# Performance work log

Measured on AMD Instinct MI355X. Metric: run time of the kernel, lower is better.

## Reference

```python
import jax, jax.numpy as jnp
import numpy as np

B, S, DM, H, D = 2, 1024, 1024, 16, 64  # batch, seq, d_model, heads, head_dim


def setup_inputs() -> dict:
    key = jax.random.key(0)
    ks = jax.random.split(key, 16)
    sc = 1.0 / np.sqrt(DM)
    scd = 1.0 / np.sqrt(D)
    return {
        "hidden_states": jax.random.normal(ks[0], (B, S, DM), dtype=jnp.float32),
        # frozen base_attn projections
        "Wq": jax.random.normal(ks[1], (DM, DM), dtype=jnp.float32) * sc,
        "bq": jnp.zeros((DM,), dtype=jnp.float32),
        "Wk": jax.random.normal(ks[2], (DM, DM), dtype=jnp.float32) * sc,
        "bk": jnp.zeros((DM,), dtype=jnp.float32),
        "Wv": jax.random.normal(ks[3], (DM, DM), dtype=jnp.float32) * sc,
        "bv": jnp.zeros((DM,), dtype=jnp.float32),
        "Wo": jax.random.normal(ks[4], (DM, DM), dtype=jnp.float32) * sc,
        "bo": jnp.zeros((DM,), dtype=jnp.float32),
        # trainable hedgehog feature maps (per-head Linear(head_dim, head_dim))
        "Wfq": jax.random.normal(ks[5], (D, D), dtype=jnp.float32) * scd,
        "bfq": jnp.zeros((D,), dtype=jnp.float32),
        "Wfk": jax.random.normal(ks[6], (D, D), dtype=jnp.float32) * scd,
        "bfk": jnp.zeros((D,), dtype=jnp.float32),
    }


def _heads(x):
    # (B, S, DM) -> (B, H, S, D)
    return x.reshape(B, S, H, D).transpose(0, 2, 1, 3)


def _feature_map(x, W, b):
    # HedgehogFeatureMap: Linear then concat(exp(x), exp(-x)) along last dim
    y = jnp.einsum('bhsd,ed->bhse', x, W) + b
    return jnp.concatenate([jnp.exp(y), jnp.exp(-y)], axis=-1)  # (B,H,S,2D)


def reference(hidden_states, Wq, bq, Wk, bk, Wv, bv, Wo, bo, Wfq, bfq, Wfk, bfk):
    # base_attn: standard multi-head softmax attention with output_attentions=True
    q = _heads(hidden_states @ Wq.T + bq)
    k = _heads(hidden_states @ Wk.T + bk)
    v = _heads(hidden_states @ Wv.T + bv)
    scores = jnp.einsum('bhmd,bhnd->bhmn', q, k) / jnp.sqrt(jnp.float32(D))
    true_attns = jax.nn.softmax(scores, axis=-1)  # (B,H,S,S)
    ctx = jnp.einsum('bhmn,bhnd->bhmd', true_attns, v)
    outputs = ctx.transpose(0, 2, 1, 3).reshape(B, S, DM) @ Wo.T + bo

    # hedgehog path: feature maps on q/k then sum-normalized quadratic attention
    fq = _feature_map(q, Wfq, bfq)
    fk = _feature_map(k, Wfk, bfk)
    qk = jnp.einsum('bhmd,bhnd->bhmn', fq, fk)
    pred_attns = qk / jnp.sum(qk, axis=-1, keepdims=True)
    return (outputs, pred_attns, true_attns)
```

## Files before the change

### kernel.cpp

```cpp
#include <hip/hip_runtime.h>
#include <math.h>

constexpr int B_ = 2, S_ = 1024, DM_ = 1024, NH_ = 16, HD_ = 64;
constexpr long SD = (long)S_ * DM_;
constexpr long SS = (long)S_ * S_;

typedef _Float16 half8 __attribute__((ext_vector_type(8)));
typedef _Float16 half4 __attribute__((ext_vector_type(4)));
typedef float floatx4 __attribute__((ext_vector_type(4)));

__device__ __forceinline__ void gl_lds16(const void* g, void* l) {
    __builtin_amdgcn_global_load_lds(
        (const __attribute__((address_space(1))) void*)g,
        (__attribute__((address_space(3))) void*)l, 16, 0, 0);
}

__device__ __forceinline__ void nt_store4(const floatx4& v, float* p) {
    __builtin_nontemporal_store(v, (floatx4*)p);
}

__global__ __launch_bounds__(256) void cvt_all(
    const float* __restrict__ hs,  const float* __restrict__ Wq,
    const float* __restrict__ Wk,  const float* __restrict__ Wv,
    const float* __restrict__ Wo,  const float* __restrict__ Wfq,
    const float* __restrict__ Wfk,
    _Float16* __restrict__ hsH, _Float16* __restrict__ WqH,
    _Float16* __restrict__ WkH, _Float16* __restrict__ WvH,
    _Float16* __restrict__ WoH, _Float16* __restrict__ WfqH,
    _Float16* __restrict__ WfkH)
{
    long i = (long)blockIdx.x * 256 + threadIdx.x;
    const float* src; _Float16* dst; long off;
    if (i < 524288)       { src = hs;  dst = hsH;  off = i; }
    else if (i < 786432)  { src = Wq;  dst = WqH;  off = i - 524288; }
    else if (i < 1048576) { src = Wk;  dst = WkH;  off = i - 786432; }
    else if (i < 1310720) { src = Wv;  dst = WvH;  off = i - 1048576; }
    else if (i < 1572864) { src = Wo;  dst = WoH;  off = i - 1310720; }
    else if (i < 1573888) { src = Wfq; dst = WfqH; off = i - 1572864; }
    else                  { src = Wfk; dst = WfkH; off = i - 1573888; }
    float4 v = ((const float4*)src)[off];
    half4 h = { (_Float16)v.x, (_Float16)v.y, (_Float16)v.z, (_Float16)v.w };
    ((half4*)dst)[off] = h;
}

template <int BM, int BN, int WM, int WN>
__global__ __launch_bounds__(256) void mm_nt(
    const _Float16* __restrict__ Ap, const _Float16* __restrict__ Wp,
    const float* __restrict__ bias, const float* __restrict__ skp,
    float* __restrict__ Cf,
    _Float16* __restrict__ Ch, int K, int lda, int ldw, int ldc,
    long sAb, long sAh, long sWb, long sWh, long sCb, long sCh,
    float scale, int mode)
{
    constexpr int MI = WM / 16, NI = WN / 16;
    const int z = blockIdx.z, b = z / NH_, h = z % NH_;
    const int wave = threadIdx.x >> 6, lane = threadIdx.x & 63;
    const int m0 = blockIdx.y * BM, n0 = blockIdx.x * BN;
    const int wm = (wave >> 1) * WM, wn = (wave & 1) * WN;
    const int r16 = lane & 15, quad = lane >> 4;

    const _Float16* Az = Ap + (long)b * sAb + (long)h * sAh;
    const _Float16* Wz = Wp + (long)b * sWb + (long)h * sWh;

    __shared__ __align__(16) _Float16 As[2 * BM * 32];
    __shared__ __align__(16) _Float16 Bs[2 * BN * 32];
    __shared__ float skz[128];
    __shared__ float rsinvs[BM];

    if (skp) {
        if (threadIdx.x < 128) {
            float s = 0.f;
#pragma unroll
            for (int m = 0; m < 16; ++m)
                s += skp[((long)z * 16 + m) * 128 + threadIdx.x];
            skz[threadIdx.x] = s;
        }
        __syncthreads();
        if (threadIdx.x < BM) {
            const _Float16* p = Az + (long)(m0 + threadIdx.x) * lda;
            float acc = 0.f;
#pragma unroll
            for (int d0 = 0; d0 < 128; d0 += 8) {
                half8 v = *(const half8*)(p + d0);
#pragma unroll
                for (int j = 0; j < 8; ++j)
                    acc = fmaf((float)v[j], skz[d0 + j], acc);
            }
            rsinvs[threadIdx.x] = 1.f / acc;
        }
    }

    floatx4 acc[MI][NI];
#pragma unroll
    for (int i = 0; i < MI; ++i)
#pragma unroll
        for (int j = 0; j < NI; ++j)
#pragma unroll
            for (int r = 0; r < 4; ++r) acc[i][j][r] = 0.f;

    for (int k0 = 0; k0 < K; k0 += 64) {
#pragma unroll
        for (int hf = 0; hf < 2; ++hf) {
#pragma unroll
            for (int c = wave * (BM / 64); c < (wave + 1) * (BM / 64); ++c) {
                const _Float16* g = Az + (long)(m0 + c * 16 + (lane >> 2)) * lda
                                    + k0 + hf * 32 + (lane & 3) * 8;
                gl_lds16(g, &As[hf * BM * 32 + c * 512]);
            }
#pragma unroll
            for (int c = wave * (BN / 64); c < (wave + 1) * (BN / 64); ++c) {
                const _Float16* g = Wz + (long)(n0 + c * 16 + (lane >> 2)) * ldw
                                    + k0 + hf * 32 + (lane & 3) * 8;
                gl_lds16(g, &Bs[hf * BN * 32 + c * 512]);
            }
        }
        __syncthreads();

#pragma unroll
        for (int hf = 0; hf < 2; ++hf) {
            half8 af[MI], bf8[NI];
#pragma unroll
            for (int i = 0; i < MI; ++i)
                af[i] = *(const half8*)&As[hf * BM * 32
                                           + (wm + i * 16 + r16) * 32 + quad * 8];
#pragma unroll
            for (int j = 0; j < NI; ++j)
                bf8[j] = *(const half8*)&Bs[hf * BN * 32
                                            + (wn + j * 16 + r16) * 32 + quad * 8];
#pragma unroll
            for (int i = 0; i < MI; ++i)
#pragma unroll
                for (int j = 0; j < NI; ++j)
                    acc[i][j] = __builtin_amdgcn_mfma_f32_16x16x32_f16(
                        bf8[j], af[i], acc[i][j], 0, 0, 0);
        }
        __syncthreads();
    }

    const long cb = (long)b * sCb + (long)h * sCh;
#pragma unroll
    for (int i = 0; i < MI; ++i) {
        const int row = m0 + wm + i * 16 + r16;
        const float rs = skp ? rsinvs[row - m0] : 1.f;
#pragma unroll
        for (int j = 0; j < NI; ++j) {
            const int col = n0 + wn + j * 16 + quad * 4;
            floatx4 v;
#pragma unroll
            for (int r = 0; r < 4; ++r) v[r] = acc[i][j][r] * scale;
            if (bias) {
                float4 bv = *(const float4*)&bias[col];
                v[0] += bv.x; v[1] += bv.y; v[2] += bv.z; v[3] += bv.w;
            }
            if (skp) {
#pragma unroll
                for (int r = 0; r < 4; ++r) v[r] *= rs;
            }
            if (mode == 0) {
                nt_store4(v, &Cf[cb + (long)row * ldc + col]);
            } else {
                half4 hv = { (_Float16)v[0], (_Float16)v[1],
                             (_Float16)v[2], (_Float16)v[3] };
                *(half4*)&Ch[cb + (long)row * ldc + col] = hv;
            }
        }
    }
}

__global__ __launch_bounds__(256) void qkv_proj(
    const _Float16* __restrict__ hsH,
    const _Float16* __restrict__ W0, const _Float16* __restrict__ W1,
    const _Float16* __restrict__ W2,
    const float* __restrict__ b0, const float* __restrict__ b1,
    const float* __restrict__ b2,
    _Float16* __restrict__ QH, _Float16* __restrict__ KH,
    _Float16* __restrict__ VtH)
{
    const int z = blockIdx.z;
    const _Float16* W = (z == 0) ? W0 : (z == 1) ? W1 : W2;
    const float* bias = (z == 0) ? b0 : (z == 1) ? b1 : b2;

    const int wave = threadIdx.x >> 6, lane = threadIdx.x & 63;
    const int m0 = blockIdx.y * 64, n0 = blockIdx.x * 128;
    const int wm = (wave >> 1) * 32, wn = (wave & 1) * 64;
    const int r16 = lane & 15, quad = lane >> 4;

    __shared__ __align__(16) _Float16 As[2 * 64 * 32];
    __shared__ __align__(16) _Float16 Bs[2 * 128 * 32];

    floatx4 acc[2][4];
#pragma unroll
    for (int i = 0; i < 2; ++i)
#pragma unroll
        for (int j = 0; j < 4; ++j)
#pragma unroll
            for (int r = 0; r < 4; ++r) acc[i][j][r] = 0.f;

    for (int k0 = 0; k0 < 1024; k0 += 64) {
#pragma unroll
        for (int hf = 0; hf < 2; ++hf) {
            const _Float16* ga = hsH + (long)(m0 + wave * 16 + (lane >> 2)) * 1024
                                 + k0 + hf * 32 + (lane & 3) * 8;
            gl_lds16(ga, &As[hf * 2048 + wave * 512]);
#pragma unroll
            for (int c = wave * 2; c < wave * 2 + 2; ++c) {
                const _Float16* gb = W + (long)(n0 + c * 16 + (lane >> 2)) * 1024
                                     + k0 + hf * 32 + (lane & 3) * 8;
                gl_lds16(gb, &Bs[hf * 4096 + c * 512]);
            }
        }
        __syncthreads();

#pragma unroll
        for (int hf = 0; hf < 2; ++hf) {
            half8 af[2], bf8[4];
#pragma unroll
            for (int i = 0; i < 2; ++i)
                af[i] = *(const half8*)&As[hf * 2048
                                           + (wm + i * 16 + r16) * 32 + quad * 8];
#pragma unroll
            for (int j = 0; j < 4; ++j)
                bf8[j] = *(const half8*)&Bs[hf * 4096
                                            + (wn + j * 16 + r16) * 32 + quad * 8];
#pragma unroll
            for (int i = 0; i < 2; ++i)
#pragma unroll
                for (int j = 0; j < 4; ++j)
                    acc[i][j] = __builtin_amdgcn_mfma_f32_16x16x32_f16(
                        bf8[j], af[i], acc[i][j], 0, 0, 0);
        }
        __syncthreads();
    }

    _Float16* dst = (z == 0) ? QH : KH;
#pragma unroll
    for (int i = 0; i < 2; ++i) {
        const int row = m0 + wm + i * 16 + r16;
#pragma unroll
        for (int j = 0; j < 4; ++j) {
            const int col = n0 + wn + j * 16 + quad * 4;
            float4 bv = *(const float4*)&bias[col];
            float v0 = acc[i][j][0] + bv.x, v1 = acc[i][j][1] + bv.y;
            float v2 = acc[i][j][2] + bv.z, v3 = acc[i][j][3] + bv.w;
            if (z < 2) {
                half4 hv = { (_Float16)v0, (_Float16)v1,
                             (_Float16)v2, (_Float16)v3 };
                *(half4*)&dst[(long)row * 1024 + col] = hv;
            } else {
                const int bb = row >> 10, s = row & 1023;
                const int hh = col >> 6, d0 = col & 63;
                float vv[4] = { v0, v1, v2, v3 };
#pragma unroll
                for (int r = 0; r < 4; ++r)
                    VtH[((((long)bb * 16 + hh) * 64 + d0 + r) << 10) | s] =
                        (_Float16)vv[r];
            }
        }
    }
}

__global__ __launch_bounds__(512) void attn_fused(
    const _Float16* __restrict__ Q, const _Float16* __restrict__ K,
    const _Float16* __restrict__ Vt, float* __restrict__ trueA,
    _Float16* __restrict__ ctx)
{
    const int z = blockIdx.y, b = z >> 4, h = z & 15;
    const int m0 = blockIdx.x * 32;
    const int wave = threadIdx.x >> 6, lane = threadIdx.x & 63;
    const int r16 = lane & 15, quad = lane >> 4;
    const int c0 = wave * 128;

    __shared__ __align__(16) _Float16 Ps[32 * 1024];
    float* redmx = (float*)Ps;
    float* redsm = (float*)Ps + 256;

    const _Float16* Qb = Q + (long)b * SD + h * 64;
    const _Float16* Kb = K + (long)b * SD + h * 64;

    half8 qf[2][2];
#pragma unroll
    for (int mi = 0; mi < 2; ++mi)
#pragma unroll
        for (int ks = 0; ks < 2; ++ks)
            qf[mi][ks] = *(const half8*)&Qb[(long)(m0 + mi * 16 + r16) * DM_
                                            + ks * 32 + quad * 8];

    floatx4 acc[2][8];
#pragma unroll
    for (int mi = 0; mi < 2; ++mi)
#pragma unroll
        for (int nj = 0; nj < 8; ++nj)
#pragma unroll
            for (int r = 0; r < 4; ++r) acc[mi][nj][r] = 0.f;

#pragma unroll
    for (int ks = 0; ks < 2; ++ks) {
#pragma unroll
        for (int nj = 0; nj < 8; ++nj) {
            half8 kf = *(const half8*)&Kb[(long)(c0 + nj * 16 + r16) * DM_
                                          + ks * 32 + quad * 8];
            acc[0][nj] = __builtin_amdgcn_mfma_f32_16x16x32_f16(
                kf, qf[0][ks], acc[0][nj], 0, 0, 0);
            acc[1][nj] = __builtin_amdgcn_mfma_f32_16x16x32_f16(
                kf, qf[1][ks], acc[1][nj], 0, 0, 0);
        }
    }

    float mxl[2];
#pragma unroll
    for (int mi = 0; mi < 2; ++mi) {
        float m = acc[mi][0][0];
#pragma unroll
        for (int nj = 0; nj < 8; ++nj)
#pragma unroll
            for (int r = 0; r < 4; ++r) m = fmaxf(m, acc[mi][nj][r]);
        m = fmaxf(m, __shfl_xor(m, 16, 64));
        m = fmaxf(m, __shfl_xor(m, 32, 64));
        mxl[mi] = m;
    }
    if (quad == 0) {
        redmx[wave * 32 + r16]      = mxl[0];
        redmx[wave * 32 + 16 + r16] = mxl[1];
    }
    __syncthreads();
    float mx[2];
#pragma unroll
    for (int mi = 0; mi < 2; ++mi) {
        float m = redmx[mi * 16 + r16];
#pragma unroll
        for (int w = 1; w < 8; ++w)
            m = fmaxf(m, redmx[w * 32 + mi * 16 + r16]);
        mx[mi] = m;
    }

    float sml[2];
#pragma unroll
    for (int mi = 0; mi < 2; ++mi) {
        float s = 0.f;
#pragma unroll
        for (int nj = 0; nj < 8; ++nj)
#pragma unroll
            for (int r = 0; r < 4; ++r) {
                float p = __expf((acc[mi][nj][r] - mx[mi]) * 0.125f);
                acc[mi][nj][r] = p;
                s += p;
            }
        s += __shfl_xor(s, 16, 64);
        s += __shfl_xor(s, 32, 64);
        sml[mi] = s;
    }
    if (quad == 0) {
        redsm[wave * 32 + r16]      = sml[0];
        redsm[wave * 32 + 16 + r16] = sml[1];
    }
    __syncthreads();
    float inv[2];
#pragma unroll
    for (int mi = 0; mi < 2; ++mi) {
        float s = 0.f;
#pragma unroll
        for (int w = 0; w < 8; ++w) s += redsm[w * 32 + mi * 16 + r16];
        inv[mi] = 1.f / s;
    }
    __syncthreads();

    float* Ta = trueA + (long)z * SS + (long)m0 * S_;
    const int sw = (r16 & 7) << 3;
#pragma unroll
    for (int mi = 0; mi < 2; ++mi) {
        const int row = mi * 16 + r16;
        const float iv = inv[mi];
#pragma unroll
        for (int nj = 0; nj < 8; ++nj) {
            const int col = c0 + nj * 16 + quad * 4;
            floatx4 tv; half4 hv;
#pragma unroll
            for (int r = 0; r < 4; ++r) {
                float v = acc[mi][nj][r] * iv;
                tv[r] = v;
                hv[r] = (_Float16)v;
            }
            nt_store4(tv, &Ta[(long)row * S_ + col]);
            *(half4*)&Ps[row * 1024 + (col ^ sw)] = hv;
        }
    }
    __syncthreads();

    const int mi = wave >> 2, d0 = (wave & 3) * 16;
    const _Float16* Vb = Vt + ((long)z * 64 + d0 + r16) * (long)S_;
    floatx4 c2;
#pragma unroll
    for (int r = 0; r < 4; ++r) c2[r] = 0.f;

    const int swz = (r16 & 7) << 3;
#pragma unroll 8
    for (int k0 = 0; k0 < 1024; k0 += 32) {
        half8 pa = *(const half8*)&Ps[(mi * 16 + r16) * 1024
                                      + ((k0 + quad * 8) ^ swz)];
        half8 vf = *(const half8*)&Vb[k0 + quad * 8];
        c2 = __builtin_amdgcn_mfma_f32_16x16x32_f16(vf, pa, c2, 0, 0, 0);
    }

    _Float16* Cb = ctx + (long)b * SD + h * 64;
    half4 cv = { (_Float16)c2[0], (_Float16)c2[1],
                 (_Float16)c2[2], (_Float16)c2[3] };
    *(half4*)&Cb[(long)(m0 + mi * 16 + r16) * DM_ + d0 + quad * 4] = cv;
}

__global__ __launch_bounds__(256) void feat_map2(
    const _Float16* __restrict__ QH, const _Float16* __restrict__ KH,
    const _Float16* __restrict__ Wfq, const _Float16* __restrict__ Wfk,
    const float* __restrict__ bfq, const float* __restrict__ bfk,
    _Float16* __restrict__ fqH, _Float16* __restrict__ fkH,
    float* __restrict__ skp)
{
    const int which = blockIdx.z;
    const _Float16* Xh = which ? KH : QH;
    const _Float16* Wf = which ? Wfk : Wfq;
    const float* bf    = which ? bfk : bfq;
    _Float16* outH     = which ? fkH : fqH;

    const int z = blockIdx.y, b = z >> 4, h = z & 15;
    const int mb = blockIdx.x, m0 = mb * 64;
    __shared__ float Xs[64][65];
    __shared__ float Ws[64][65];
    __shared__ float red[16][128];
    const _Float16* Xb = Xh + (long)b * SD + h * 64;
    for (int i = threadIdx.x; i < 4096; i += 256) {
        int r = i >> 6, c = i & 63;
        Xs[r][c] = (float)Xb[(long)(m0 + r) * 1024 + c];
        Ws[r][c] = (float)Wf[i];
    }
    __syncthreads();
    const int tmg = threadIdx.x >> 4;
    const int tm = tmg * 4, tn = (threadIdx.x & 15) * 4;
    float acc[4][4] = {{0.f}};
    for (int k = 0; k < 64; ++k) {
        float xv[4], wv[4];
#pragma unroll
        for (int i = 0; i < 4; ++i) xv[i] = Xs[tm + i][k];
#pragma unroll
        for (int j = 0; j < 4; ++j) wv[j] = Ws[tn + j][k];
#pragma unroll
        for (int i = 0; i < 4; ++i)
#pragma unroll
            for (int j = 0; j < 4; ++j) acc[i][j] = fmaf(xv[i], wv[j], acc[i][j]);
    }
    float sp[4] = {0.f, 0.f, 0.f, 0.f}, sn[4] = {0.f, 0.f, 0.f, 0.f};
#pragma unroll
    for (int i = 0; i < 4; ++i) {
        long base = ((long)z * S_ + m0 + tm + i) * 128;
#pragma unroll
        for (int j = 0; j < 4; ++j) {
            float y = acc[i][j] + bf[tn + j];
            float ep = expf(y), en = expf(-y);
            outH[base + tn + j]      = (_Float16)ep;
            outH[base + 64 + tn + j] = (_Float16)en;
            sp[j] += ep; sn[j] += en;
        }
    }
    if (which) {
#pragma unroll
        for (int j = 0; j < 4; ++j) {
            red[tmg][tn + j]      = sp[j];
            red[tmg][64 + tn + j] = sn[j];
        }
        __syncthreads();
        if (threadIdx.x < 128) {
            float s = 0.f;
#pragma unroll
            for (int g = 0; g < 16; ++g) s += red[g][threadIdx.x];
            skp[((long)z * 16 + mb) * 128 + threadIdx.x] = s;
        }
    }
}

extern "C" void kernel_launch(void* const* d_in, const int* in_sizes, int n_in,
                              void* d_out, int out_size, void* d_ws, size_t ws_size,
                              hipStream_t stream)
{
    (void)in_sizes; (void)n_in; (void)out_size; (void)ws_size;

    const float* hs  = (const float*)d_in[0];
    const float* Wq  = (const float*)d_in[1];
    const float* bq  = (const float*)d_in[2];
    const float* Wk  = (const float*)d_in[3];
    const float* bk  = (const float*)d_in[4];
    const float* Wv  = (const float*)d_in[5];
    const float* bv  = (const float*)d_in[6];
    const float* Wo  = (const float*)d_in[7];
    const float* bo  = (const float*)d_in[8];
    const float* Wfq = (const float*)d_in[9];
    const float* bfq = (const float*)d_in[10];
    const float* Wfk = (const float*)d_in[11];
    const float* bfk = (const float*)d_in[12];

    float* out0  = (float*)d_out;
    float* pred  = out0 + (long)B_ * S_ * DM_;
    float* trueA = pred + (long)B_ * NH_ * S_ * S_;

    _Float16* hsH  = (_Float16*)d_ws;
    _Float16* WqH  = hsH + 2 * 1024 * 1024;
    _Float16* WkH  = WqH + 1024 * 1024;
    _Float16* WvH  = WkH + 1024 * 1024;
    _Float16* WoH  = WvH + 1024 * 1024;
    _Float16* WfqH = WoH + 1024 * 1024;
    _Float16* WfkH = WfqH + 4096;
    _Float16* QH   = WfkH + 4096;
    _Float16* KH   = QH + 2 * 1024 * 1024;
    _Float16* VtH  = KH + 2 * 1024 * 1024;
    _Float16* ctxH = VtH + 2 * 1024 * 1024;
    _Float16* fqH  = ctxH + 2 * 1024 * 1024;
    _Float16* fkH  = fqH + (long)B_ * NH_ * S_ * 128;

    float* skp = (float*)WqH;

    const dim3 blk(256);

    cvt_all<<<6152, blk, 0, stream>>>(
        hs, Wq, Wk, Wv, Wo, Wfq, Wfk,
        hsH, WqH, WkH, WvH, WoH, WfqH, WfkH);

    qkv_proj<<<dim3(8, 32, 3), blk, 0, stream>>>(
        hsH, WqH, WkH, WvH, bq, bk, bv, QH, KH, VtH);

    attn_fused<<<dim3(32, 32), dim3(512), 0, stream>>>(
        QH, KH, VtH, trueA, ctxH);

    mm_nt<64, 64, 32, 32><<<dim3(16, 32, 1), blk, 0, stream>>>(
        ctxH, WoH, bo, nullptr, out0, nullptr, 1024, 1024, 1024, 1024,
        0, 0, 0, 0, 0, 0, 1.f, 0);

    feat_map2<<<dim3(16, 32, 2), blk, 0, stream>>>(
        QH, KH, WfqH, WfkH, bfq, bfk, fqH, fkH, skp);

    mm_nt<128, 128, 64, 64><<<dim3(8, 8, 32), blk, 0, stream>>>(
        fqH, fkH, nullptr, skp, pred, nullptr, 128, 128, 128, 1024,
        (long)16 * S_ * 128, (long)S_ * 128,
        (long)16 * S_ * 128, (long)S_ * 128,
        16 * SS, SS, 1.f, 0);
}
```

Measured before the change: 448.8 us.

## Shrink attention blocks to 16 rows and merge output projection with feature maps

The attention kernel now uses 256-thread blocks that each own 16 query rows, with each wave covering 256 key columns. That doubles the grid and halves LDS per block, which should raise occupancy. The output projection GEMM and the hedgehog feature-map kernel are merged into a single launch that branches on block index, so one kernel launch goes away and the two independent jobs can overlap on the GPU. In exchange, the merged kernel reserves the larger shared-memory size for every block, and the new inline GEMM has no pipelining.

```diff
diff --git a/kernel.cpp b/kernel.cpp
--- a/kernel.cpp
+++ b/kernel.cpp
@@ -259,134 +259,97 @@
     }
 }
 
-__global__ __launch_bounds__(512) void attn_fused(
+__global__ __launch_bounds__(256) void attn_fused(
     const _Float16* __restrict__ Q, const _Float16* __restrict__ K,
     const _Float16* __restrict__ Vt, float* __restrict__ trueA,
     _Float16* __restrict__ ctx)
 {
     const int z = blockIdx.y, b = z >> 4, h = z & 15;
-    const int m0 = blockIdx.x * 32;
+    const int m0 = blockIdx.x * 16;
     const int wave = threadIdx.x >> 6, lane = threadIdx.x & 63;
     const int r16 = lane & 15, quad = lane >> 4;
-    const int c0 = wave * 128;
-
-    __shared__ __align__(16) _Float16 Ps[32 * 1024];
+    const int c0 = wave * 256;
+
+    __shared__ __align__(16) _Float16 Ps[16 * 1024];
     float* redmx = (float*)Ps;
-    float* redsm = (float*)Ps + 256;
+    float* redsm = (float*)Ps + 64;
 
     const _Float16* Qb = Q + (long)b * SD + h * 64;
     const _Float16* Kb = K + (long)b * SD + h * 64;
 
-    half8 qf[2][2];
-#pragma unroll
-    for (int mi = 0; mi < 2; ++mi)
-#pragma unroll
-        for (int ks = 0; ks < 2; ++ks)
-            qf[mi][ks] = *(const half8*)&Qb[(long)(m0 + mi * 16 + r16) * DM_
-                                            + ks * 32 + quad * 8];
-
-    floatx4 acc[2][8];
-#pragma unroll
-    for (int mi = 0; mi < 2; ++mi)
-#pragma unroll
-        for (int nj = 0; nj < 8; ++nj)
-#pragma unroll
-            for (int r = 0; r < 4; ++r) acc[mi][nj][r] = 0.f;
+    half8 qf[2];
+#pragma unroll
+    for (int ks = 0; ks < 2; ++ks)
+        qf[ks] = *(const half8*)&Qb[(long)(m0 + r16) * DM_ + ks * 32 + quad * 8];
+
+    floatx4 acc[16];
+#pragma unroll
+    for (int nj = 0; nj < 16; ++nj)
+#pragma unroll
+        for (int r = 0; r < 4; ++r) acc[nj][r] = 0.f;
 
 #pragma unroll
     for (int ks = 0; ks < 2; ++ks) {
 #pragma unroll
-        for (int nj = 0; nj < 8; ++nj) {
+        for (int nj = 0; nj < 16; ++nj) {
             half8 kf = *(const half8*)&Kb[(long)(c0 + nj * 16 + r16) * DM_
                                           + ks * 32 + quad * 8];
-            acc[0][nj] = __builtin_amdgcn_mfma_f32_16x16x32_f16(
-                kf, qf[0][ks], acc[0][nj], 0, 0, 0);
-            acc[1][nj] = __builtin_amdgcn_mfma_f32_16x16x32_f16(
-                kf, qf[1][ks], acc[1][nj], 0, 0, 0);
-        }
-    }
-
-    float mxl[2];
-#pragma unroll
-    for (int mi = 0; mi < 2; ++mi) {
-        float m = acc[mi][0][0];
-#pragma unroll
-        for (int nj = 0; nj < 8; ++nj)
-#pragma unroll
-            for (int r = 0; r < 4; ++r) m = fmaxf(m, acc[mi][nj][r]);
+            acc[nj] = __builtin_amdgcn_mfma_f32_16x16x32_f16(
+                kf, qf[ks], acc[nj], 0, 0, 0);
+        }
+    }
+
+    {
+        float m = acc[0][0];
+#pragma unroll
+        for (int nj = 0; nj < 16; ++nj)
+#pragma unroll
+            for (int r = 0; r < 4; ++r) m = fmaxf(m, acc[nj][r]);
         m = fmaxf(m, __shfl_xor(m, 16, 64));
         m = fmaxf(m, __shfl_xor(m, 32, 64));
-        mxl[mi] = m;
-    }
-    if (quad == 0) {
-        redmx[wave * 32 + r16]      = mxl[0];
-        redmx[wave * 32 + 16 + r16] = mxl[1];
+        if (quad == 0) redmx[wave * 16 + r16] = m;
     }
     __syncthreads();
-    float mx[2];
-#pragma unroll
-    for (int mi = 0; mi < 2; ++mi) {
-        float m = redmx[mi * 16 + r16];
-#pragma unroll
-        for (int w = 1; w < 8; ++w)
-            m = fmaxf(m, redmx[w * 32 + mi * 16 + r16]);
-        mx[mi] = m;
-    }
-
-    float sml[2];
-#pragma unroll
-    for (int mi = 0; mi < 2; ++mi) {
+    float mx = fmaxf(fmaxf(redmx[r16], redmx[16 + r16]),
+                     fmaxf(redmx[32 + r16], redmx[48 + r16]));
+
+    {
         float s = 0.f;
 #pragma unroll
-        for (int nj = 0; nj < 8; ++nj)
+        for (int nj = 0; nj < 16; ++nj)
 #pragma unroll
             for (int r = 0; r < 4; ++r) {
-                float p = __expf((acc[mi][nj][r] - mx[mi]) * 0.125f);
-                acc[mi][nj][r] = p;
+                float p = __expf((acc[nj][r] - mx) * 0.125f);
+                acc[nj][r] = p;
                 s += p;
             }
         s += __shfl_xor(s, 16, 64);
         s += __shfl_xor(s, 32, 64);
-        sml[mi] = s;
-    }
-    if (quad == 0) {
-        redsm[wave * 32 + r16]      = sml[0];
-        redsm[wave * 32 + 16 + r16] = sml[1];
+        if (quad == 0) redsm[wave * 16 + r16] = s;
     }
     __syncthreads();
-    float inv[2];
-#pragma unroll
-    for (int mi = 0; mi < 2; ++mi) {
-        float s = 0.f;
-#pragma unroll
-        for (int w = 0; w < 8; ++w) s += redsm[w * 32 + mi * 16 + r16];
-        inv[mi] = 1.f / s;
-    }
+    const float inv = 1.f / (redsm[r16] + redsm[16 + r16]
+                             + redsm[32 + r16] + redsm[48 + r16]);
     __syncthreads();
 
     float* Ta = trueA + (long)z * SS + (long)m0 * S_;
     const int sw = (r16 & 7) << 3;
 #pragma unroll
-    for (int mi = 0; mi < 2; ++mi) {
-        const int row = mi * 16 + r16;
-        const float iv = inv[mi];
-#pragma unroll
-        for (int nj = 0; nj < 8; ++nj) {
-            const int col = c0 + nj * 16 + quad * 4;
-            floatx4 tv; half4 hv;
-#pragma unroll
-            for (int r = 0; r < 4; ++r) {
-                float v = acc[mi][nj][r] * iv;
-                tv[r] = v;
-                hv[r] = (_Float16)v;
-            }
-            nt_store4(tv, &Ta[(long)row * S_ + col]);
-            *(half4*)&Ps[row * 1024 + (col ^ sw)] = hv;
-        }
+    for (int nj = 0; nj < 16; ++nj) {
+        const int col = c0 + nj * 16 + quad * 4;
+        floatx4 tv; half4 hv;
+#pragma unroll
+        for (int r = 0; r < 4; ++r) {
+            float v = acc[nj][r] * inv;
+            tv[r] = v;
+            hv[r] = (_Float16)v;
+        }
+        nt_store4(tv, &Ta[(long)r16 * S_ + col]);
+        *(half4*)&Ps[r16 * 1024 + (col ^ sw)] = hv;
     }
     __syncthreads();
 
-    const int mi = wave >> 2, d0 = (wave & 3) * 16;
+    const int d0 = wave * 16;
     const _Float16* Vb = Vt + ((long)z * 64 + d0 + r16) * (long)S_;
     floatx4 c2;
 #pragma unroll
@@ -395,8 +358,7 @@
     const int swz = (r16 & 7) << 3;
 #pragma unroll 8
     for (int k0 = 0; k0 < 1024; k0 += 32) {
-        half8 pa = *(const half8*)&Ps[(mi * 16 + r16) * 1024
-                                      + ((k0 + quad * 8) ^ swz)];
+        half8 pa = *(const half8*)&Ps[r16 * 1024 + ((k0 + quad * 8) ^ swz)];
         half8 vf = *(const half8*)&Vb[k0 + quad * 8];
         c2 = __builtin_amdgcn_mfma_f32_16x16x32_f16(vf, pa, c2, 0, 0, 0);
     }
@@ -404,73 +366,146 @@
     _Float16* Cb = ctx + (long)b * SD + h * 64;
     half4 cv = { (_Float16)c2[0], (_Float16)c2[1],
                  (_Float16)c2[2], (_Float16)c2[3] };
-    *(half4*)&Cb[(long)(m0 + mi * 16 + r16) * DM_ + d0 + quad * 4] = cv;
-}
-
-__global__ __launch_bounds__(256) void feat_map2(
+    *(half4*)&Cb[(long)(m0 + r16) * DM_ + d0 + quad * 4] = cv;
+}
+
+__global__ __launch_bounds__(256) void tail_fused(
+    const _Float16* __restrict__ ctxH, const _Float16* __restrict__ WoH,
+    const float* __restrict__ bo, float* __restrict__ out0,
     const _Float16* __restrict__ QH, const _Float16* __restrict__ KH,
     const _Float16* __restrict__ Wfq, const _Float16* __restrict__ Wfk,
     const float* __restrict__ bfq, const float* __restrict__ bfk,
     _Float16* __restrict__ fqH, _Float16* __restrict__ fkH,
     float* __restrict__ skp)
 {
-    const int which = blockIdx.z;
-    const _Float16* Xh = which ? KH : QH;
-    const _Float16* Wf = which ? Wfk : Wfq;
-    const float* bf    = which ? bfk : bfq;
-    _Float16* outH     = which ? fkH : fqH;
-
-    const int z = blockIdx.y, b = z >> 4, h = z & 15;
-    const int mb = blockIdx.x, m0 = mb * 64;
-    __shared__ float Xs[64][65];
-    __shared__ float Ws[64][65];
-    __shared__ float red[16][128];
-    const _Float16* Xb = Xh + (long)b * SD + h * 64;
-    for (int i = threadIdx.x; i < 4096; i += 256) {
-        int r = i >> 6, c = i & 63;
-        Xs[r][c] = (float)Xb[(long)(m0 + r) * 1024 + c];
-        Ws[r][c] = (float)Wf[i];
-    }
-    __syncthreads();
-    const int tmg = threadIdx.x >> 4;
-    const int tm = tmg * 4, tn = (threadIdx.x & 15) * 4;
-    float acc[4][4] = {{0.f}};
-    for (int k = 0; k < 64; ++k) {
-        float xv[4], wv[4];
-#pragma unroll
-        for (int i = 0; i < 4; ++i) xv[i] = Xs[tm + i][k];
-#pragma unroll
-        for (int j = 0; j < 4; ++j) wv[j] = Ws[tn + j][k];
-#pragma unroll
-        for (int i = 0; i < 4; ++i)
-#pragma unroll
-            for (int j = 0; j < 4; ++j) acc[i][j] = fmaf(xv[i], wv[j], acc[i][j]);
-    }
-    float sp[4] = {0.f, 0.f, 0.f, 0.f}, sn[4] = {0.f, 0.f, 0.f, 0.f};
-#pragma unroll
-    for (int i = 0; i < 4; ++i) {
-        long base = ((long)z * S_ + m0 + tm + i) * 128;
-#pragma unroll
-        for (int j = 0; j < 4; ++j) {
-            float y = acc[i][j] + bf[tn + j];
-            float ep = expf(y), en = expf(-y);
-            outH[base + tn + j]      = (_Float16)ep;
-            outH[base + 64 + tn + j] = (_Float16)en;
-            sp[j] += ep; sn[j] += en;
-        }
-    }
-    if (which) {
-#pragma unroll
-        for (int j = 0; j < 4; ++j) {
-            red[tmg][tn + j]      = sp[j];
-            red[tmg][64 + tn + j] = sn[j];
+    __shared__ __align__(16) char smem[41472];
+    const int bid = blockIdx.x;
+
+    if (bid < 512) {
+        _Float16* As = (_Float16*)smem;
+        _Float16* Bs = (_Float16*)(smem + 8192);
+        const int bx = bid & 15, by = bid >> 4;
+        const int wave = threadIdx.x >> 6, lane = threadIdx.x & 63;
+        const int m0 = by * 64, n0 = bx * 64;
+        const int wm = (wave >> 1) * 32, wn = (wave & 1) * 32;
+        const int r16 = lane & 15, quad = lane >> 4;
+
+        floatx4 acc[2][2];
+#pragma unroll
+        for (int i = 0; i < 2; ++i)
+#pragma unroll
+            for (int j = 0; j < 2; ++j)
+#pragma unroll
+                for (int r = 0; r < 4; ++r) acc[i][j][r] = 0.f;
+
+        for (int k0 = 0; k0 < 1024; k0 += 64) {
+#pragma unroll
+            for (int hf = 0; hf < 2; ++hf) {
+                const _Float16* ga = ctxH + (long)(m0 + wave * 16 + (lane >> 2)) * 1024
+                                     + k0 + hf * 32 + (lane & 3) * 8;
+                gl_lds16(ga, &As[hf * 2048 + wave * 512]);
+                const _Float16* gb = WoH + (long)(n0 + wave * 16 + (lane >> 2)) * 1024
+                                     + k0 + hf * 32 + (lane & 3) * 8;
+                gl_lds16(gb, &Bs[hf * 2048 + wave * 512]);
+            }
+            __syncthreads();
+#pragma unroll
+            for (int hf = 0; hf < 2; ++hf) {
+                half8 af[2], bf8[2];
+#pragma unroll
+                for (int i = 0; i < 2; ++i)
+                    af[i] = *(const half8*)&As[hf * 2048
+                                               + (wm + i * 16 + r16) * 32 + quad * 8];
+#pragma unroll
+                for (int j = 0; j < 2; ++j)
+                    bf8[j] = *(const half8*)&Bs[hf * 2048
+                                                + (wn + j * 16 + r16) * 32 + quad * 8];
+#pragma unroll
+                for (int i = 0; i < 2; ++i)
+#pragma unroll
+                    for (int j = 0; j < 2; ++j)
+                        acc[i][j] = __builtin_amdgcn_mfma_f32_16x16x32_f16(
+                            bf8[j], af[i], acc[i][j], 0, 0, 0);
+            }
+            __syncthreads();
+        }
+
+#pragma unroll
+        for (int i = 0; i < 2; ++i) {
+            const int row = m0 + wm + i * 16 + r16;
+#pragma unroll
+            for (int j = 0; j < 2; ++j) {
+                const int col = n0 + wn + j * 16 + quad * 4;
+                float4 bv = *(const float4*)&bo[col];
+                floatx4 v;
+                v[0] = acc[i][j][0] + bv.x; v[1] = acc[i][j][1] + bv.y;
+                v[2] = acc[i][j][2] + bv.z; v[3] = acc[i][j][3] + bv.w;
+                nt_store4(v, &out0[(long)row * 1024 + col]);
+            }
+        }
+    } else {
+        const int fid = bid - 512;
+        const int which = fid >> 9;
+        const int z = (fid >> 4) & 31, mb = fid & 15;
+        const _Float16* Xh = which ? KH : QH;
+        const _Float16* Wf = which ? Wfk : Wfq;
+        const float* bf    = which ? bfk : bfq;
+        _Float16* outH     = which ? fkH : fqH;
+
+        float (*Xs)[65] = (float(*)[65])smem;
+        float (*Ws)[65] = (float(*)[65])(smem + 16640);
+        float (*red)[128] = (float(*)[128])(smem + 33280);
+
+        const int b = z >> 4, h = z & 15;
+        const int m0 = mb * 64;
+        const _Float16* Xb = Xh + (long)b * SD + h * 64;
+        for (int i = threadIdx.x; i < 4096; i += 256) {
+            int r = i >> 6, c = i & 63;
+            Xs[r][c] = (float)Xb[(long)(m0 + r) * 1024 + c];
+            Ws[r][c] = (float)Wf[i];
         }
         __syncthreads();
-        if (threadIdx.x < 128) {
-            float s = 0.f;
-#pragma unroll
-            for (int g = 0; g < 16; ++g) s += red[g][threadIdx.x];
-            skp[((long)z * 16 + mb) * 128 + threadIdx.x] = s;
+        const int tmg = threadIdx.x >> 4;
+        const int tm = tmg * 4, tn = (threadIdx.x & 15) * 4;
+        float acc[4][4] = {{0.f}};
+        for (int k = 0; k < 64; ++k) {
+            float xv[4], wv[4];
+#pragma unroll
+            for (int i = 0; i < 4; ++i) xv[i] = Xs[tm + i][k];
+#pragma unroll
+            for (int j = 0; j < 4; ++j) wv[j] = Ws[tn + j][k];
+#pragma unroll
+            for (int i = 0; i < 4; ++i)
+#pragma unroll
+                for (int j = 0; j < 4; ++j)
+                    acc[i][j] = fmaf(xv[i], wv[j], acc[i][j]);
+        }
+        float sp[4] = {0.f, 0.f, 0.f, 0.f}, sn[4] = {0.f, 0.f, 0.f, 0.f};
+#pragma unroll
+        for (int i = 0; i < 4; ++i) {
+            long base = ((long)z * S_ + m0 + tm + i) * 128;
+#pragma unroll
+            for (int j = 0; j < 4; ++j) {
+                float y = acc[i][j] + bf[tn + j];
+                float ep = expf(y), en = expf(-y);
+                outH[base + tn + j]      = (_Float16)ep;
+                outH[base + 64 + tn + j] = (_Float16)en;
+                sp[j] += ep; sn[j] += en;
+            }
+        }
+        if (which) {
+#pragma unroll
+            for (int j = 0; j < 4; ++j) {
+                red[tmg][tn + j]      = sp[j];
+                red[tmg][64 + tn + j] = sn[j];
+            }
+            __syncthreads();
+            if (threadIdx.x < 128) {
+                float s = 0.f;
+#pragma unroll
+                for (int g = 0; g < 16; ++g) s += red[g][threadIdx.x];
+                skp[((long)z * 16 + mb) * 128 + threadIdx.x] = s;
+            }
         }
     }
 }
@@ -524,14 +559,11 @@
     qkv_proj<<<dim3(8, 32, 3), blk, 0, stream>>>(
         hsH, WqH, WkH, WvH, bq, bk, bv, QH, KH, VtH);
 
-    attn_fused<<<dim3(32, 32), dim3(512), 0, stream>>>(
+    attn_fused<<<dim3(64, 32), blk, 0, stream>>>(
         QH, KH, VtH, trueA, ctxH);
 
-    mm_nt<64, 64, 32, 32><<<dim3(16, 32, 1), blk, 0, stream>>>(
-        ctxH, WoH, bo, nullptr, out0, nullptr, 1024, 1024, 1024, 1024,
-        0, 0, 0, 0, 0, 0, 1.f, 0);
-
-    feat_map2<<<dim3(16, 32, 2), blk, 0, stream>>>(
+    tail_fused<<<1536, blk, 0, stream>>>(
+        ctxH, WoH, bo, out0,
         QH, KH, WfqH, WfkH, bfq, bfk, fqH, fkH, skp);
 
     mm_nt<128, 128, 64, 64><<<dim3(8, 8, 32), blk, 0, stream>>>(
```

Result: faster. 438.5 us (-2.3%).
